# Performance work log

Measured on AMD Instinct MI355X. Metric: run time of the kernel, lower is better.

## Reference

```python
import jax, jax.numpy as jnp
import numpy as np

N_NODES = 50000
N_EDGES = 640000
D_IN = 128
D_HID = 128
D_OUT = 128
N_GRAPHS = 64


def gcn_conv(x, edge_index, W, b, n_nodes):
    """PyG GCNConv: D^{-1/2} (A + I) D^{-1/2} X W + b (unit edge weights)."""
    src, dst = edge_index[0], edge_index[1]
    h = x @ W  # [N, d_out]
    # degree counts target-side edges plus the self loop
    deg = jax.ops.segment_sum(jnp.ones_like(dst, dtype=h.dtype), dst,
                              num_segments=n_nodes) + 1.0
    dinv = jax.lax.rsqrt(deg)  # deg >= 1 so always finite
    norm = dinv[src] * dinv[dst]  # [E]
    msg = h[src] * norm[:, None]  # gather + scale  [E, d_out]
    agg = jax.ops.segment_sum(msg, dst, num_segments=n_nodes)
    # self-loop contribution: norm_ii = dinv_i^2
    agg = agg + h * (dinv * dinv)[:, None]
    return agg + b


def global_mean_pool(x, batch, n_graphs):
    sums = jax.ops.segment_sum(x, batch, num_segments=n_graphs)
    cnt = jax.ops.segment_sum(jnp.ones((x.shape[0],), dtype=x.dtype), batch,
                              num_segments=n_graphs)
    return sums / jnp.maximum(cnt, 1.0)[:, None]


def setup_inputs() -> dict:
    key = jax.random.key(0)
    k = jax.random.split(key, 8)
    x = jax.random.normal(k[0], (N_NODES, D_IN), dtype=jnp.float32)
    edge_index = jax.random.randint(k[1], (2, N_EDGES), 0, N_NODES, dtype=jnp.int64)
    batch = jnp.sort(jax.random.randint(k[2], (N_NODES,), 0, N_GRAPHS, dtype=jnp.int64))
    s1 = 1.0 / np.sqrt(D_IN)
    s2 = 1.0 / np.sqrt(D_HID)
    W1 = jax.random.uniform(k[3], (D_IN, D_HID), jnp.float32, -s1, s1)
    b1 = jnp.zeros((D_HID,), jnp.float32)
    W2 = jax.random.uniform(k[4], (D_HID, D_OUT), jnp.float32, -s2, s2)
    b2 = jnp.zeros((D_OUT,), jnp.float32)
    return {"x": x, "edge_index": edge_index, "batch": batch,
            "W1": W1, "b1": b1, "W2": W2, "b2": b2}


def reference(x, edge_index, batch, W1, b1, W2, b2):
    n = x.shape[0]
    h = jax.nn.relu(gcn_conv(x, edge_index, W1, b1, n))
    h = gcn_conv(h, edge_index, W2, b2, n)
    return global_mean_pool(h, batch, N_GRAPHS)
```

## Files before the change

kernel.cpp:

```cpp
#include <hip/hip_runtime.h>


#define D 128
#define NGRAPH 64
#define AGG_BLOCKS 2048
#define BUCK_SH 9
#define BUCK_W  512
#define MAXBUCK 128

typedef _Float16 h16x2 __attribute__((ext_vector_type(2)));
typedef _Float16 f16x8 __attribute__((ext_vector_type(8)));
typedef float    f32x4 __attribute__((ext_vector_type(4)));
typedef unsigned short u16x8 __attribute__((ext_vector_type(8)));

__device__ __forceinline__ float2 h2f(unsigned u) {
    h16x2 h = __builtin_bit_cast(h16x2, u);
    return make_float2((float)h.x, (float)h.y);
}
__device__ __forceinline__ unsigned f2h(float x, float y) {
    h16x2 h;
    h.x = (_Float16)x;
    h.y = (_Float16)y;
    return __builtin_bit_cast(unsigned, h);
}

__global__ void zero_out_kernel(float* __restrict__ out, int n) {
    int i = blockIdx.x * blockDim.x + threadIdx.x;
    if (i < n) out[i] = 0.f;
}

__global__ __launch_bounds__(256) void pack_scatter_kernel(const float* __restrict__ W1,
                                                           _Float16* __restrict__ WB,
                                                           const int* __restrict__ ei,
                                                           int* __restrict__ bcnt,
                                                           unsigned* __restrict__ buck,
                                                           unsigned* __restrict__ Gz,
                                                           unsigned* __restrict__ Hz,
                                                           int N, int E, int CAP) {
    int b = (int)blockIdx.x;
    int t = (int)threadIdx.x;
    if (b < 8) {
        int idx = b * 256 + t;
        int lane = idx & 63;
        int nt   = (idx >> 6) & 7;
        int kt   = idx >> 9;
        int col  = nt * 16 + (lane & 15);
        int krow = kt * 32 + (lane >> 4) * 8;
#pragma unroll
        for (int j = 0; j < 8; ++j)
            WB[idx * 8 + j] = (_Float16)W1[(krow + j) * D + col];
        return;
    }
    if (b == 8) {
        if (t < 64)       Gz[(size_t)N * 64 + t] = 0u;
        else if (t < 128) Hz[(size_t)N * 64 + (t - 64)] = 0u;
        return;
    }
    __shared__ unsigned histL[MAXBUCK];
    __shared__ int      baseL[MAXBUCK];
    if (t < MAXBUCK) histL[t] = 0u;
    __syncthreads();

    int e0 = (b - 9) * 1024;
    int bid[4];
    unsigned lidx[4], pk[4];
#pragma unroll
    for (int j = 0; j < 4; ++j) {
        int e = e0 + t + j * 256;
        bid[j] = -1;
        if (e < E) {
            int s = ei[e];
            int d = ei[E + e];
            if (d >= 0 && d < N) {
                s = min(max(s, 0), N - 1);
                bid[j] = d >> BUCK_SH;
                pk[j]  = ((unsigned)d << 16) | (unsigned)s;
            }
        }
    }
#pragma unroll
    for (int j = 0; j < 4; ++j)
        if (bid[j] >= 0) lidx[j] = atomicAdd(&histL[bid[j]], 1u);
    __syncthreads();
    if (t < MAXBUCK && histL[t] > 0u)
        baseL[t] = atomicAdd(&bcnt[t], (int)histL[t]);
    __syncthreads();
#pragma unroll
    for (int j = 0; j < 4; ++j)
        if (bid[j] >= 0) {
            int slot = baseL[bid[j]] + (int)lidx[j];
            if (slot < CAP) buck[(size_t)bid[j] * CAP + slot] = pk[j];
        }
}

__global__ __launch_bounds__(256) void bucket_deg_kernel(const unsigned* __restrict__ buck,
                                                         const int* __restrict__ bcnt,
                                                         int* __restrict__ deg,
                                                         float* __restrict__ dinv,
                                                         int* __restrict__ padsum,
                                                         int* __restrict__ bbase,
                                                         int* __restrict__ rowstart,
                                                         int* __restrict__ ticket,
                                                         int N, int CAP, int nbuck) {
    __shared__ int degL[BUCK_W];
    __shared__ int red[256];
    __shared__ int lastFlag;
    int b = (int)blockIdx.x;
    int t = (int)threadIdx.x;
    for (int k = t; k < BUCK_W; k += 256) degL[k] = 0;
    __syncthreads();
    int cnt = min(bcnt[b], CAP);
    const unsigned* bp = buck + (size_t)b * CAP;
    for (int i = t; i < cnt; i += 256)
        atomicAdd(&degL[(bp[i] >> 16) & (BUCK_W - 1)], 1);
    __syncthreads();
    int base = b << BUCK_SH;
    int local = 0;
    for (int k = t; k < BUCK_W; k += 256) {
        int d = base + k;
        if (d < N) {
            int dg = degL[k];
            deg[d]  = dg;
            dinv[d] = rsqrtf((float)dg + 1.0f);
            local  += (dg + 7) & ~7;
        }
    }
    red[t] = local;
    __syncthreads();
    for (int off = 128; off > 0; off >>= 1) {
        if (t < off) red[t] += red[t + off];
        __syncthreads();
    }
    if (t == 0) padsum[b] = red[0];
    __threadfence();
    if (t == 0) lastFlag = (atomicAdd(ticket, 1) == nbuck - 1) ? 1 : 0;
    __syncthreads();
    if (lastFlag) {
        __threadfence();
        __shared__ int s[128];
        int own = (t < nbuck) ? padsum[t] : 0;
        if (t < 128) s[t] = own;
        __syncthreads();
        for (int off = 1; off < 128; off <<= 1) {
            int v = (t < 128 && t >= off) ? s[t - off] : 0;
            __syncthreads();
            if (t < 128) s[t] += v;
            __syncthreads();
        }
        if (t < nbuck) bbase[t] = s[t] - own;
        if (t == 127) rowstart[N] = s[127];
    }
}

__global__ __launch_bounds__(256) void gemm_fill_kernel(const float* __restrict__ X,
                                                        const _Float16* __restrict__ WB,
                                                        const float* __restrict__ dinv,
                                                        _Float16* __restrict__ Gh,
                                                        const unsigned* __restrict__ buck,
                                                        const int* __restrict__ bcnt,
                                                        const int* __restrict__ deg,
                                                        const int* __restrict__ bbase,
                                                        int* __restrict__ rowstart,
                                                        unsigned short* __restrict__ colidx,
                                                        int N, int CAP, int gb) {
    if ((int)blockIdx.x >= gb) {
        __shared__ int degS[BUCK_W];
        __shared__ int loff[BUCK_W];
        __shared__ int sc[256];
        int b = (int)blockIdx.x - gb;
        int t = (int)threadIdx.x;
        int base_d = b << BUCK_SH;
        for (int k = t; k < BUCK_W; k += 256) {
            int d = base_d + k;
            degS[k] = (d < N) ? deg[d] : 0;
        }
        __syncthreads();
        int p0 = (degS[2 * t] + 7) & ~7;
        int p1 = (degS[2 * t + 1] + 7) & ~7;
        int own = p0 + p1;
        sc[t] = own;
        __syncthreads();
        for (int off = 1; off < 256; off <<= 1) {
            int v = (t >= off) ? sc[t - off] : 0;
            __syncthreads();
            sc[t] += v;
            __syncthreads();
        }
        int excl = sc[t] - own;
        loff[2 * t]     = excl;
        loff[2 * t + 1] = excl + p0;
        __syncthreads();
        int bb = bbase[b];
        for (int k = t; k < BUCK_W; k += 256) {
            int d = base_d + k;
            if (d < N) {
                int rs = bb + loff[k];
                rowstart[d] = rs;
                int dg = degS[k];
                int p8 = (dg + 7) & ~7;
                for (int j = dg; j < p8; ++j)
                    colidx[rs + j] = (unsigned short)N;
            }
        }
        __syncthreads();
        for (int k = t; k < BUCK_W; k += 256) degS[k] = bb + loff[k];
        __syncthreads();
        int cnt = min(bcnt[b], CAP);
        const unsigned* bp = buck + (size_t)b * CAP;
        for (int i = t; i < cnt; i += 256) {
            unsigned u = bp[i];
            int ld = (int)((u >> 16) & (BUCK_W - 1));
            int slot = atomicAdd(&degS[ld], 1);
            colidx[slot] = (unsigned short)(u & 0xffffu);
        }
        return;
    }

    int t = (int)threadIdx.x;
    int wave = t >> 6, lane = t & 63;
    int mbase = blockIdx.x * 64 + wave * 16;
    int arow  = mbase + (lane & 15);
    if (arow >= N) arow = N - 1;
    int kgrp  = lane >> 4;

    f16x8 afrag[4];
#pragma unroll
    for (int kt = 0; kt < 4; ++kt) {
        const float* xp = X + (size_t)arow * D + kt * 32 + kgrp * 8;
        float4 a0 = *(const float4*)xp;
        float4 a1 = *(const float4*)(xp + 4);
        f16x8 af;
        af[0] = (_Float16)a0.x; af[1] = (_Float16)a0.y;
        af[2] = (_Float16)a0.z; af[3] = (_Float16)a0.w;
        af[4] = (_Float16)a1.x; af[5] = (_Float16)a1.y;
        af[6] = (_Float16)a1.z; af[7] = (_Float16)a1.w;
        afrag[kt] = af;
    }
    f32x4 acc[8];
#pragma unroll
    for (int nt = 0; nt < 8; ++nt) acc[nt] = (f32x4){0.f, 0.f, 0.f, 0.f};
#pragma unroll
    for (int kt = 0; kt < 4; ++kt) {
#pragma unroll
        for (int nt = 0; nt < 8; ++nt) {
            uint4 u = *(const uint4*)(WB + (((kt * 8 + nt) * 64 + lane) * 8));
            f16x8 bfrag = __builtin_bit_cast(f16x8, u);
            acc[nt] = __builtin_amdgcn_mfma_f32_16x16x32_f16(bfrag, afrag[kt], acc[nt], 0, 0, 0);
        }
    }
    int row = mbase + (lane & 15);
    if (row < N) {
        float dv = dinv[row];
#pragma unroll
        for (int nt = 0; nt < 8; ++nt) {
            uint2 w;
            w.x = f2h(dv * acc[nt][0], dv * acc[nt][1]);
            w.y = f2h(dv * acc[nt][2], dv * acc[nt][3]);
            *(uint2*)(Gh + (size_t)row * D + nt * 16 + kgrp * 4) = w;
        }
    }
}

__global__ __launch_bounds__(256) void agg1_kernel(const unsigned* __restrict__ Gh,
                                                   const int* __restrict__ rowstart,
                                                   const unsigned short* __restrict__ colidx,
                                                   const float* __restrict__ dinv,
                                                   const float* __restrict__ b1,
                                                   unsigned* __restrict__ Hh,
                                                   int N, int chunk) {
    int gid  = blockIdx.x * 4 + (threadIdx.x >> 6);
    unsigned lane = threadIdx.x & 63;
    int i0 = gid * chunk, i1 = min(i0 + chunk, N);
    float bx = b1[2 * lane], by = b1[2 * lane + 1];
    for (int i = i0; i < i1; ++i) {
        float di = dinv[i];
        float2 acc = h2f(Gh[((unsigned)i << 6) + lane]);
        int e0 = rowstart[i], e1 = rowstart[i + 1];
        for (int e = e0; e < e1; e += 8) {
            u16x8 cc = *(const u16x8*)(colidx + e);
            unsigned u[8];
#pragma unroll
            for (int j = 0; j < 8; ++j)
                u[j] = Gh[((unsigned)cc[j] << 6) + lane];
#pragma unroll
            for (int j = 0; j < 8; ++j) {
                float2 v = h2f(u[j]);
                acc.x += v.x;
                acc.y += v.y;
            }
        }
        float hx = fmaxf(fmaf(di, acc.x, bx), 0.f) * di;
        float hy = fmaxf(fmaf(di, acc.y, by), 0.f) * di;
        Hh[((unsigned)i << 6) + lane] = f2h(hx, hy);
    }
}

__global__ __launch_bounds__(256) void agg2_pool_kernel(const unsigned* __restrict__ Hh,
                                                        const int* __restrict__ rowstart,
                                                        const unsigned short* __restrict__ colidx,
                                                        const float* __restrict__ dinv,
                                                        const int* __restrict__ batch,
                                                        float* __restrict__ pool,
                                                        int N, int chunk) {
    int gid  = blockIdx.x * 4 + (threadIdx.x >> 6);
    unsigned lane = threadIdx.x & 63;
    int i0 = gid * chunk, i1 = min(i0 + chunk, N);
    if (i0 >= N) return;

    float2 pa = make_float2(0.f, 0.f);
    int cur = min(max(batch[i0], 0), NGRAPH - 1);
    for (int i = i0; i < i1; ++i) {
        float di = dinv[i];
        float2 a = h2f(Hh[((unsigned)i << 6) + lane]);
        int e0 = rowstart[i], e1 = rowstart[i + 1];
        for (int e = e0; e < e1; e += 8) {
            u16x8 cc = *(const u16x8*)(colidx + e);
            unsigned u[8];
#pragma unroll
            for (int j = 0; j < 8; ++j)
                u[j] = Hh[((unsigned)cc[j] << 6) + lane];
#pragma unroll
            for (int j = 0; j < 8; ++j) {
                float2 v = h2f(u[j]);
                a.x += v.x;
                a.y += v.y;
            }
        }
        int b = min(max(batch[i], 0), NGRAPH - 1);
        if (b != cur) {
            atomicAdd(&pool[(size_t)cur * D + 2 * lane], pa.x);
            atomicAdd(&pool[(size_t)cur * D + 2 * lane + 1], pa.y);
            pa = make_float2(0.f, 0.f);
            cur = b;
        }
        pa.x = fmaf(di, a.x, pa.x);
        pa.y = fmaf(di, a.y, pa.y);
    }
    atomicAdd(&pool[(size_t)cur * D + 2 * lane], pa.x);
    atomicAdd(&pool[(size_t)cur * D + 2 * lane + 1], pa.y);
}

__device__ __forceinline__ int lbound(const int* __restrict__ a, int n, int v) {
    int lo = 0, hi = n;
    while (lo < hi) {
        int m = (lo + hi) >> 1;
        if (a[m] < v) lo = m + 1; else hi = m;
    }
    return lo;
}

__global__ void final_gemm_kernel(const float* __restrict__ pool,
                                  const int* __restrict__ batch,
                                  const float* __restrict__ W2,
                                  const float* __restrict__ b2,
                                  float* __restrict__ out, int N) {
    int g = blockIdx.x, o = threadIdx.x;
    int s = lbound(batch, N, g);
    int e = lbound(batch, N, g + 1);
    float inv_cnt = 1.0f / fmaxf((float)(e - s), 1.0f);
    float acc = 0.f;
#pragma unroll 4
    for (int k = 0; k < D; ++k)
        acc = fmaf(pool[g * D + k], W2[k * D + o], acc);
    out[g * D + o] = acc * inv_cnt + b2[o];
}


extern "C" void kernel_launch(void* const* d_in, const int* in_sizes, int n_in,
                              void* d_out, int out_size, void* d_ws, size_t ws_size,
                              hipStream_t stream) {
    const float* x     = (const float*)d_in[0];
    const int*   ei    = (const int*)  d_in[1];
    const int*   batch = (const int*)  d_in[2];
    const float* W1    = (const float*)d_in[3];
    const float* b1    = (const float*)d_in[4];
    const float* W2    = (const float*)d_in[5];
    const float* b2    = (const float*)d_in[6];
    float* out = (float*)d_out;

    const int N = in_sizes[0] / D;
    const int E = in_sizes[1] / 2;
    const int nbuck = (N + BUCK_W - 1) >> BUCK_SH;
    const int CAP   = (E / (nbuck > 0 ? nbuck : 1)) * 2 + 1024;

    char* ws = (char*)d_ws;
    size_t off = 0;
    auto carve = [&](size_t bytes) {
        size_t o = off;
        off = (off + bytes + 255) & ~(size_t)255;
        return o;
    };
    size_t o_bcnt     = carve((size_t)MAXBUCK * 4);
    size_t o_pool     = carve((size_t)NGRAPH * D * 4);
    size_t o_ticket   = carve((size_t)256);
    size_t zspan      = off;
    size_t o_rowstart = carve((size_t)(N + 1) * 4);
    size_t o_deg      = carve((size_t)N * 4);
    size_t o_dinv     = carve((size_t)N * 4);
    size_t o_padsum   = carve((size_t)MAXBUCK * 4);
    size_t o_bbase    = carve((size_t)MAXBUCK * 4);
    size_t o_colidx   = carve(((size_t)E + 7 * (size_t)N + 64) * 2);
    size_t o_buck     = carve((size_t)nbuck * CAP * 4);
    size_t o_wb       = carve((size_t)D * D * 2);
    size_t o_gh       = carve((size_t)(N + 1) * D * 2);
    size_t o_hh       = carve((size_t)(N + 1) * D * 2);
    size_t need = off;

    if (ws_size < need) {
        zero_out_kernel<<<(out_size + 255) / 256, 256, 0, stream>>>(out, out_size);
        return;
    }

    int*            bcnt     = (int*)           (ws + o_bcnt);
    float*          pool     = (float*)         (ws + o_pool);
    int*            ticket   = (int*)           (ws + o_ticket);
    int*            rowstart = (int*)           (ws + o_rowstart);
    int*            deg      = (int*)           (ws + o_deg);
    float*          dinv     = (float*)         (ws + o_dinv);
    int*            padsum   = (int*)           (ws + o_padsum);
    int*            bbase    = (int*)           (ws + o_bbase);
    unsigned short* colidx   = (unsigned short*)(ws + o_colidx);
    unsigned*       buck     = (unsigned*)      (ws + o_buck);
    _Float16*       WB       = (_Float16*)      (ws + o_wb);
    _Float16*       Gh       = (_Float16*)      (ws + o_gh);
    _Float16*       Hh       = (_Float16*)      (ws + o_hh);

    hipMemsetAsync(ws, 0, zspan, stream);

    int ebs = (E + 1023) / 1024;
    int gb  = (N + 63) / 64;

    pack_scatter_kernel<<<9 + ebs, 256, 0, stream>>>(W1, WB, ei, bcnt, buck,
                                                     (unsigned*)Gh, (unsigned*)Hh,
                                                     N, E, CAP);
    bucket_deg_kernel<<<nbuck, 256, 0, stream>>>(buck, bcnt, deg, dinv, padsum,
                                                 bbase, rowstart, ticket,
                                                 N, CAP, nbuck);
    gemm_fill_kernel<<<gb + nbuck, 256, 0, stream>>>(x, WB, dinv, Gh, buck, bcnt,
                                                     deg, bbase, rowstart, colidx,
                                                     N, CAP, gb);

    int groups = AGG_BLOCKS * 4;
    int chunk  = (N + groups - 1) / groups;
    agg1_kernel<<<AGG_BLOCKS, 256, 0, stream>>>((const unsigned*)Gh, rowstart, colidx,
                                                dinv, b1, (unsigned*)Hh, N, chunk);
    agg2_pool_kernel<<<AGG_BLOCKS, 256, 0, stream>>>((const unsigned*)Hh, rowstart, colidx,
                                                     dinv, batch, pool, N, chunk);
    final_gemm_kernel<<<NGRAPH, D, 0, stream>>>(pool, batch, W2, b2, out, N);
}
```

Measured before the change: 206.4 us.

## Halve bucket width, put CSR-fill blocks first, and swap MFMA operand order

Bucket width drops from 512 to 256 destination nodes, which doubles the bucket count to 256 and gives one node per thread in the degree and fill kernels. The CSR-fill blocks are moved ahead of the GEMM blocks in the combined launch, so the slower scatter work is scheduled first. The MFMA operands are swapped so each lane now holds per-row outputs, and the epilogue writes individual fp16 elements instead of packed uint2 stores. The trade-off is more buckets with fewer edges each, and narrower, less vectorized stores of Gh.

```diff
diff --git a/kernel.cpp b/kernel.cpp
--- a/kernel.cpp
+++ b/kernel.cpp
@@ -4,9 +4,9 @@
 #define D 128
 #define NGRAPH 64
 #define AGG_BLOCKS 2048
-#define BUCK_SH 9
-#define BUCK_W  512
-#define MAXBUCK 128
+#define BUCK_SH 8
+#define BUCK_W  256
+#define MAXBUCK 256
 
 typedef _Float16 h16x2 __attribute__((ext_vector_type(2)));
 typedef _Float16 f16x8 __attribute__((ext_vector_type(8)));
@@ -58,7 +58,7 @@
     }
     __shared__ unsigned histL[MAXBUCK];
     __shared__ int      baseL[MAXBUCK];
-    if (t < MAXBUCK) histL[t] = 0u;
+    histL[t] = 0u;
     __syncthreads();
 
     int e0 = (b - 9) * 1024;
@@ -82,7 +82,7 @@
     for (int j = 0; j < 4; ++j)
         if (bid[j] >= 0) lidx[j] = atomicAdd(&histL[bid[j]], 1u);
     __syncthreads();
-    if (t < MAXBUCK && histL[t] > 0u)
+    if (histL[t] > 0u)
         baseL[t] = atomicAdd(&bcnt[t], (int)histL[t]);
     __syncthreads();
 #pragma unroll
@@ -107,7 +107,7 @@
     __shared__ int lastFlag;
     int b = (int)blockIdx.x;
     int t = (int)threadIdx.x;
-    for (int k = t; k < BUCK_W; k += 256) degL[k] = 0;
+    degL[t] = 0;
     __syncthreads();
     int cnt = min(bcnt[b], CAP);
     const unsigned* bp = buck + (size_t)b * CAP;
@@ -115,15 +115,13 @@
         atomicAdd(&degL[(bp[i] >> 16) & (BUCK_W - 1)], 1);
     __syncthreads();
     int base = b << BUCK_SH;
+    int d = base + t;
     int local = 0;
-    for (int k = t; k < BUCK_W; k += 256) {
-        int d = base + k;
-        if (d < N) {
-            int dg = degL[k];
-            deg[d]  = dg;
-            dinv[d] = rsqrtf((float)dg + 1.0f);
-            local  += (dg + 7) & ~7;
-        }
+    if (d < N) {
+        int dg = degL[t];
+        deg[d]  = dg;
+        dinv[d] = rsqrtf((float)dg + 1.0f);
+        local   = (dg + 7) & ~7;
     }
     red[t] = local;
     __syncthreads();
@@ -137,18 +135,18 @@
     __syncthreads();
     if (lastFlag) {
         __threadfence();
-        __shared__ int s[128];
+        __shared__ int s[256];
         int own = (t < nbuck) ? padsum[t] : 0;
-        if (t < 128) s[t] = own;
+        s[t] = own;
         __syncthreads();
-        for (int off = 1; off < 128; off <<= 1) {
-            int v = (t < 128 && t >= off) ? s[t - off] : 0;
+        for (int off = 1; off < 256; off <<= 1) {
+            int v = (t >= off) ? s[t - off] : 0;
             __syncthreads();
-            if (t < 128) s[t] += v;
+            s[t] += v;
             __syncthreads();
         }
         if (t < nbuck) bbase[t] = s[t] - own;
-        if (t == 127) rowstart[N] = s[127];
+        if (t == 255) rowstart[N] = s[255];
     }
 }
 
@@ -162,23 +160,17 @@
                                                         const int* __restrict__ bbase,
                                                         int* __restrict__ rowstart,
                                                         unsigned short* __restrict__ colidx,
-                                                        int N, int CAP, int gb) {
-    if ((int)blockIdx.x >= gb) {
-        __shared__ int degS[BUCK_W];
-        __shared__ int loff[BUCK_W];
+                                                        int N, int CAP, int nbuck) {
+    int t = (int)threadIdx.x;
+    if ((int)blockIdx.x < nbuck) {
+        __shared__ int curS[BUCK_W];
         __shared__ int sc[256];
-        int b = (int)blockIdx.x - gb;
-        int t = (int)threadIdx.x;
+        int b = (int)blockIdx.x;
         int base_d = b << BUCK_SH;
-        for (int k = t; k < BUCK_W; k += 256) {
-            int d = base_d + k;
-            degS[k] = (d < N) ? deg[d] : 0;
-        }
-        __syncthreads();
-        int p0 = (degS[2 * t] + 7) & ~7;
-        int p1 = (degS[2 * t + 1] + 7) & ~7;
-        int own = p0 + p1;
-        sc[t] = own;
+        int d = base_d + t;
+        int dg = (d < N) ? deg[d] : 0;
+        int p8 = (dg + 7) & ~7;
+        sc[t] = p8;
         __syncthreads();
         for (int off = 1; off < 256; off <<= 1) {
             int v = (t >= off) ? sc[t - off] : 0;
@@ -186,39 +178,28 @@
             sc[t] += v;
             __syncthreads();
         }
-        int excl = sc[t] - own;
-        loff[2 * t]     = excl;
-        loff[2 * t + 1] = excl + p0;
-        __syncthreads();
-        int bb = bbase[b];
-        for (int k = t; k < BUCK_W; k += 256) {
-            int d = base_d + k;
-            if (d < N) {
-                int rs = bb + loff[k];
-                rowstart[d] = rs;
-                int dg = degS[k];
-                int p8 = (dg + 7) & ~7;
-                for (int j = dg; j < p8; ++j)
-                    colidx[rs + j] = (unsigned short)N;
-            }
-        }
-        __syncthreads();
-        for (int k = t; k < BUCK_W; k += 256) degS[k] = bb + loff[k];
+        int rs = bbase[b] + sc[t] - p8;
+        if (d < N) {
+            rowstart[d] = rs;
+            for (int j = dg; j < p8; ++j)
+                colidx[rs + j] = (unsigned short)N;
+        }
+        curS[t] = rs;
         __syncthreads();
         int cnt = min(bcnt[b], CAP);
         const unsigned* bp = buck + (size_t)b * CAP;
         for (int i = t; i < cnt; i += 256) {
             unsigned u = bp[i];
             int ld = (int)((u >> 16) & (BUCK_W - 1));
-            int slot = atomicAdd(&degS[ld], 1);
+            int slot = atomicAdd(&curS[ld], 1);
             colidx[slot] = (unsigned short)(u & 0xffffu);
         }
         return;
     }
 
-    int t = (int)threadIdx.x;
+    int gbid = (int)blockIdx.x - nbuck;
     int wave = t >> 6, lane = t & 63;
-    int mbase = blockIdx.x * 64 + wave * 16;
+    int mbase = gbid * 64 + wave * 16;
     int arow  = mbase + (lane & 15);
     if (arow >= N) arow = N - 1;
     int kgrp  = lane >> 4;
@@ -245,18 +226,18 @@
         for (int nt = 0; nt < 8; ++nt) {
             uint4 u = *(const uint4*)(WB + (((kt * 8 + nt) * 64 + lane) * 8));
             f16x8 bfrag = __builtin_bit_cast(f16x8, u);
-            acc[nt] = __builtin_amdgcn_mfma_f32_16x16x32_f16(bfrag, afrag[kt], acc[nt], 0, 0, 0);
-        }
-    }
-    int row = mbase + (lane & 15);
-    if (row < N) {
-        float dv = dinv[row];
-#pragma unroll
-        for (int nt = 0; nt < 8; ++nt) {
-            uint2 w;
-            w.x = f2h(dv * acc[nt][0], dv * acc[nt][1]);
-            w.y = f2h(dv * acc[nt][2], dv * acc[nt][3]);
-            *(uint2*)(Gh + (size_t)row * D + nt * 16 + kgrp * 4) = w;
+            acc[nt] = __builtin_amdgcn_mfma_f32_16x16x32_f16(afrag[kt], bfrag, acc[nt], 0, 0, 0);
+        }
+    }
+    int r0 = mbase + kgrp * 4;
+#pragma unroll
+    for (int r = 0; r < 4; ++r) {
+        int row = r0 + r;
+        if (row < N) {
+            float dv = dinv[row];
+#pragma unroll
+            for (int nt = 0; nt < 8; ++nt)
+                Gh[(size_t)row * D + nt * 16 + (lane & 15)] = (_Float16)(dv * acc[nt][r]);
         }
     }
 }
@@ -436,9 +417,9 @@
     bucket_deg_kernel<<<nbuck, 256, 0, stream>>>(buck, bcnt, deg, dinv, padsum,
                                                  bbase, rowstart, ticket,
                                                  N, CAP, nbuck);
-    gemm_fill_kernel<<<gb + nbuck, 256, 0, stream>>>(x, WB, dinv, Gh, buck, bcnt,
+    gemm_fill_kernel<<<nbuck + gb, 256, 0, stream>>>(x, WB, dinv, Gh, buck, bcnt,
                                                      deg, bbase, rowstart, colidx,
-                                                     N, CAP, gb);
+                                                     N, CAP, nbuck);
 
     int groups = AGG_BLOCKS * 4;
     int chunk  = (N + groups - 1) / groups;
```

Result: faster. 199.8 us (-3.2%).
